# Kernel optimization log

Measured on AMD Instinct MI355X. Metric: run time of the kernel, lower is better.

Reference implementation:

```python
import jax, jax.numpy as jnp
import numpy as np

B, T, D, H, HD, I = 256, 1, 2048, 16, 128, 5504
EPS = 1e-6
ROPE_THETA = 10000.0


def setup_inputs() -> dict:
    key = jax.random.key(0)
    ks = jax.random.split(key, 20)
    W = 0.02  # weight init scale
    hidden_states = jax.random.normal(ks[0], (B, T, D), jnp.float32)
    # RoPE tables for each batch element at a distinct decode position
    pos = jnp.arange(B, dtype=jnp.float32) % 4096.0
    inv_freq = 1.0 / (ROPE_THETA ** (jnp.arange(0, HD, 2, dtype=jnp.float32) / HD))
    ang = pos[:, None] * inv_freq[None, :]                      # [B, HD/2]
    emb = jnp.concatenate([ang, ang], axis=-1)                  # [B, HD]
    cos = jnp.cos(emb)[:, None, :]                              # [B, 1, HD]
    sin = jnp.sin(emb)[:, None, :]
    n = lambda k, s: jax.random.normal(k, s, jnp.float32) * W
    return {
        'hidden_states': hidden_states, 'cos': cos, 'sin': sin,
        'router_w': n(ks[1], (D,)), 'router_b': jnp.zeros((1,), jnp.float32),
        'ln1_w': jnp.ones((D,), jnp.float32), 'ln2_w': jnp.ones((D,), jnp.float32),
        'wq': n(ks[2], (D, D)), 'bq': jnp.zeros((D,), jnp.float32),
        'wk': n(ks[3], (D, D)), 'bk': jnp.zeros((D,), jnp.float32),
        'wv': n(ks[4], (D, D)), 'bv': jnp.zeros((D,), jnp.float32),
        'wo': n(ks[5], (D, D)),
        'w_gate': n(ks[6], (D, I)), 'w_up': n(ks[7], (D, I)), 'w_down': n(ks[8], (I, D)),
        'k_sel': 128,
    }


def _rms(x, w):
    v = jnp.mean(jnp.square(x), axis=-1, keepdims=True)
    return x * jax.lax.rsqrt(v + EPS) * w


def _rotate_half(x):
    x1, x2 = jnp.split(x, 2, axis=-1)
    return jnp.concatenate([-x2, x1], axis=-1)


def _decoder_layer(x, cs, sn, ln1_w, ln2_w, wq, bq, wk, bk, wv, bv, wo, w_gate, w_up, w_down):
    # x: [k, T, D]; cs/sn: [k, T, HD]
    k = x.shape[0]
    h = _rms(x, ln1_w)
    q = (h @ wq + bq).reshape(k, T, H, HD).transpose(0, 2, 1, 3)  # [k,H,T,HD]
    kk = (h @ wk + bk).reshape(k, T, H, HD).transpose(0, 2, 1, 3)
    v = (h @ wv + bv).reshape(k, T, H, HD).transpose(0, 2, 1, 3)
    c = cs[:, None, :, :]  # [k,1,T,HD]
    s = sn[:, None, :, :]
    q = q * c + _rotate_half(q) * s
    kk = kk * c + _rotate_half(kk) * s
    att = jnp.einsum('bhqd,bhkd->bhqk', q, kk) * (HD ** -0.5)
    p = jax.nn.softmax(att, axis=-1)  # T==1: trivial causal mask
    o = jnp.einsum('bhqk,bhkd->bhqd', p, v).transpose(0, 2, 1, 3).reshape(k, T, D) @ wo
    x = x + o
    h2 = _rms(x, ln2_w)
    mlp = (jax.nn.silu(h2 @ w_gate) * (h2 @ w_up)) @ w_down
    return x + mlp


def reference(hidden_states, cos, sin, router_w, router_b, ln1_w, ln2_w,
              wq, bq, wk, bk, wv, bv, wo, w_gate, w_up, w_down, k_sel):
    # causal router: linear D->1 scores per batch row (T==1 decode step)
    scores = hidden_states[:, 0, :] @ router_w + router_b[0]   # [B]
    probs = jax.nn.sigmoid(scores)
    _, sel_idx = jax.lax.top_k(probs, k_sel)                   # [k]
    x_sel = hidden_states[sel_idx]                             # gather [k,T,D]
    cs, sn = cos[sel_idx], sin[sel_idx]                        # [k,T,HD]
    x_out = _decoder_layer(x_sel, cs, sn, ln1_w, ln2_w, wq, bq, wk, bk,
                           wv, bv, wo, w_gate, w_up, w_down)
    return hidden_states.at[sel_idx].set(x_out)                # scatter back
```

## Files before the change

kernel.cpp:

```cpp
#include <hip/hip_runtime.h>
#include <hip/hip_bf16.h>
#include <stdint.h>


#define D_ 2048
#define I_ 5504
#define NROWS 256
#define KSEL 128

typedef __attribute__((ext_vector_type(8))) short short8;
typedef __attribute__((ext_vector_type(4))) float floatx4;

__device__ __forceinline__ unsigned short f2bf(float f) {
  union { float f; unsigned int u; } v; v.f = f;
  unsigned int r = (v.u + 0x7FFFu + ((v.u >> 16) & 1u)) >> 16;
  return (unsigned short)r;
}

__global__ void k_router(const float* __restrict__ hid, const float* __restrict__ rw,
                         const float* __restrict__ rb, float* __restrict__ scores) {
  int b = blockIdx.x, t = threadIdx.x;
  const float* x = hid + (size_t)b * D_;
  float s = 0.f;
  for (int i = t; i < D_; i += 256) s += x[i] * rw[i];
  for (int o = 32; o; o >>= 1) s += __shfl_down(s, o);
  __shared__ float red[4];
  if ((t & 63) == 0) red[t >> 6] = s;
  __syncthreads();
  if (t == 0) scores[b] = red[0] + red[1] + red[2] + red[3] + rb[0];
}

__global__ void k_select(const float* __restrict__ scores, const int* __restrict__ kptr,
                         int* __restrict__ sel, int* __restrict__ pos) {
  __shared__ float sv[NROWS];
  int t = threadIdx.x;
  sv[t] = scores[t];
  __syncthreads();
  float s = sv[t];
  int c = 0;
  for (int j = 0; j < NROWS; ++j) {
    float o = sv[j];
    c += (o > s) || (o == s && j < t);
  }
  int k = *kptr;
  if (c < k) sel[c] = t;
  pos[t] = (c < k) ? c : -1;
}

__global__ void k_rms1(const float* __restrict__ hid, const int* __restrict__ sel,
                       const float* __restrict__ ln1, const float* __restrict__ bv,
                       unsigned short* __restrict__ Hb, float* __restrict__ V,
                       float* __restrict__ X1) {
  int i = blockIdx.x, t = threadIdx.x;
  int r = sel[i];
  const float* x = hid + (size_t)r * D_;
  float xs[8]; float ss = 0.f;
#pragma unroll
  for (int c = 0; c < 8; ++c) { float v = x[t + c * 256]; xs[c] = v; ss += v * v; }
  for (int o = 32; o; o >>= 1) ss += __shfl_down(ss, o);
  __shared__ float red[4];
  if ((t & 63) == 0) red[t >> 6] = ss;
  __syncthreads();
  float inv = rsqrtf((red[0] + red[1] + red[2] + red[3]) * (1.0f / D_) + 1e-6f);
#pragma unroll
  for (int c = 0; c < 8; ++c) {
    int idx = t + c * 256;
    size_t o_ = (size_t)i * D_ + idx;
    Hb[o_] = f2bf(xs[c] * inv * ln1[idx]);
    V[o_] = bv[idx];
    X1[o_] = xs[c];
  }
}

__global__ void k_rms2(const float* __restrict__ X1, const float* __restrict__ ln2,
                       unsigned short* __restrict__ H2b, float* __restrict__ G,
                       float* __restrict__ U) {
  int i = blockIdx.x, t = threadIdx.x;
  const float* x = X1 + (size_t)i * D_;
  float xs[8]; float ss = 0.f;
#pragma unroll
  for (int c = 0; c < 8; ++c) { float v = x[t + c * 256]; xs[c] = v; ss += v * v; }
  for (int o = 32; o; o >>= 1) ss += __shfl_down(ss, o);
  __shared__ float red[4];
  if ((t & 63) == 0) red[t >> 6] = ss;
  __syncthreads();
  float inv = rsqrtf((red[0] + red[1] + red[2] + red[3]) * (1.0f / D_) + 1e-6f);
#pragma unroll
  for (int c = 0; c < 8; ++c) {
    int idx = t + c * 256;
    H2b[(size_t)i * D_ + idx] = f2bf(xs[c] * inv * ln2[idx]);
  }
  for (int j = t; j < I_; j += 256) {
    G[(size_t)i * I_ + j] = 0.f;
    U[(size_t)i * I_ + j] = 0.f;
  }
}

__global__ void k_silu_out(const float* __restrict__ G, const float* __restrict__ U,
                           unsigned short* __restrict__ Mb,
                           const float* __restrict__ X1, const int* __restrict__ pos,
                           const float* __restrict__ hid, float* __restrict__ out) {
  int tid = blockIdx.x * 256 + threadIdx.x;
  int stride = gridDim.x * 256;
  const int nM = KSEL * I_;
  for (int i = tid; i < nM; i += stride) {
    float g = G[i], u = U[i];
    float m = (g / (1.f + expf(-g))) * u;
    Mb[i] = f2bf(m);
  }
  const int nO4 = NROWS * (D_ / 4);
  const float4* X14 = (const float4*)X1;
  const float4* H4 = (const float4*)hid;
  float4* O4 = (float4*)out;
  for (int i = tid; i < nO4; i += stride) {
    int row = i >> 9;
    int c4 = i & 511;
    int p = pos[row];
    O4[i] = (p >= 0) ? X14[(size_t)p * 512 + c4] : H4[i];
  }
}

template<bool AF32, bool DUAL>
__global__ __launch_bounds__(256)
void k_gemm(const void* __restrict__ Ap, const float* __restrict__ B0,
            const float* __restrict__ B1, float* __restrict__ C0,
            float* __restrict__ C1, const int* __restrict__ rowmap,
            int K, int N, int KT, int ldc) {
  constexpr int SA = 40;
  constexpr int SB = 40;
  const int bn = blockIdx.x;
  const int kt0 = blockIdx.y * KT;
  const int kt1 = min(K, kt0 + KT);
  const int tid = threadIdx.x;
  const int lane = tid & 63;
  const int wave = tid >> 6;
  const int wm = wave >> 1, wn = wave & 1;
  const int fm = lane & 15, kq = lane >> 4;

  __shared__ alignas(16) unsigned short Asm[128 * SA];
  __shared__ alignas(16) unsigned short Bsm0[64 * SB];
  __shared__ alignas(16) unsigned short Bsm1[DUAL ? 64 * SB : 8];

  floatx4 acc0[4][2] = {};
  floatx4 acc1[4][2] = {};

  const int ar = tid >> 1;
  const int ac = (tid & 1) * 16;
  const int n2 = (tid & 31) * 2;
  const int kh = (tid >> 5) * 4;

  const unsigned short* Ab = AF32 ? nullptr : (const unsigned short*)Ap + (size_t)ar * K + ac;
  const float*          Af = AF32 ? (const float*)Ap + (size_t)ar * K + ac : nullptr;
  const float* B0b = B0 + (size_t)bn * 64 + n2;
  const float* B1b = DUAL ? B1 + (size_t)bn * 64 + n2 : nullptr;

  uint4 a16[2];
  float af32[16];
  float2 b0r[4], b1r[4];

  auto load_tile = [&](int kt) {
    if (AF32) {
#pragma unroll
      for (int r = 0; r < 4; ++r)
        *(float4*)&af32[r * 4] = *(const float4*)(Af + kt + r * 4);
    } else {
      const uint4* Ag = (const uint4*)(Ab + kt);
      a16[0] = Ag[0]; a16[1] = Ag[1];
    }
    const float* Bg0 = B0b + (size_t)(kt + kh) * N;
#pragma unroll
    for (int r = 0; r < 4; ++r) b0r[r] = *(const float2*)(Bg0 + (size_t)r * N);
    if (DUAL) {
      const float* Bg1 = B1b + (size_t)(kt + kh) * N;
#pragma unroll
      for (int r = 0; r < 4; ++r) b1r[r] = *(const float2*)(Bg1 + (size_t)r * N);
    }
  };

  load_tile(kt0);

  for (int kt = kt0; kt < kt1; kt += 32) {
    __syncthreads();
    if (AF32) {
      alignas(16) unsigned short us[16];
#pragma unroll
      for (int r = 0; r < 16; ++r) us[r] = f2bf(af32[r]);
      uint4* Ad = (uint4*)&Asm[ar * SA + ac];
      Ad[0] = ((const uint4*)us)[0]; Ad[1] = ((const uint4*)us)[1];
    } else {
      uint4* Ad = (uint4*)&Asm[ar * SA + ac];
      Ad[0] = a16[0]; Ad[1] = a16[1];
    }
    {
      unsigned long long w0 = (unsigned long long)f2bf(b0r[0].x)
                            | ((unsigned long long)f2bf(b0r[1].x) << 16)
                            | ((unsigned long long)f2bf(b0r[2].x) << 32)
                            | ((unsigned long long)f2bf(b0r[3].x) << 48);
      unsigned long long w1 = (unsigned long long)f2bf(b0r[0].y)
                            | ((unsigned long long)f2bf(b0r[1].y) << 16)
                            | ((unsigned long long)f2bf(b0r[2].y) << 32)
                            | ((unsigned long long)f2bf(b0r[3].y) << 48);
      *(unsigned long long*)&Bsm0[(n2 + 0) * SB + kh] = w0;
      *(unsigned long long*)&Bsm0[(n2 + 1) * SB + kh] = w1;
      if (DUAL) {
        unsigned long long v0 = (unsigned long long)f2bf(b1r[0].x)
                              | ((unsigned long long)f2bf(b1r[1].x) << 16)
                              | ((unsigned long long)f2bf(b1r[2].x) << 32)
                              | ((unsigned long long)f2bf(b1r[3].x) << 48);
        unsigned long long v1 = (unsigned long long)f2bf(b1r[0].y)
                              | ((unsigned long long)f2bf(b1r[1].y) << 16)
                              | ((unsigned long long)f2bf(b1r[2].y) << 32)
                              | ((unsigned long long)f2bf(b1r[3].y) << 48);
        *(unsigned long long*)&Bsm1[(n2 + 0) * SB + kh] = v0;
        *(unsigned long long*)&Bsm1[(n2 + 1) * SB + kh] = v1;
      }
    }
    __syncthreads();
    if (kt + 32 < kt1) load_tile(kt + 32);
    short8 afr[4], bf0[2], bf1[2];
#pragma unroll
    for (int i = 0; i < 4; ++i)
      afr[i] = *(const short8*)&Asm[(wm * 64 + i * 16 + fm) * SA + kq * 8];
#pragma unroll
    for (int j = 0; j < 2; ++j)
      bf0[j] = *(const short8*)&Bsm0[(wn * 32 + j * 16 + fm) * SB + kq * 8];
    if (DUAL) {
#pragma unroll
      for (int j = 0; j < 2; ++j)
        bf1[j] = *(const short8*)&Bsm1[(wn * 32 + j * 16 + fm) * SB + kq * 8];
    }
#pragma unroll
    for (int i = 0; i < 4; ++i) {
#pragma unroll
      for (int j = 0; j < 2; ++j) {
        acc0[i][j] = __builtin_amdgcn_mfma_f32_16x16x32_bf16(afr[i], bf0[j], acc0[i][j], 0, 0, 0);
        if (DUAL)
          acc1[i][j] = __builtin_amdgcn_mfma_f32_16x16x32_bf16(afr[i], bf1[j], acc1[i][j], 0, 0, 0);
      }
    }
  }

#pragma unroll
  for (int i = 0; i < 4; ++i) {
#pragma unroll
    for (int r = 0; r < 4; ++r) {
      int row = wm * 64 + i * 16 + kq * 4 + r;
      size_t rbase = rowmap ? (size_t)rowmap[row] * ldc : (size_t)row * ldc;
#pragma unroll
      for (int j = 0; j < 2; ++j) {
        int col = bn * 64 + wn * 32 + j * 16 + fm;
        atomicAdd(&C0[rbase + col], acc0[i][j][r]);
        if (DUAL) atomicAdd(&C1[rbase + col], acc1[i][j][r]);
      }
    }
  }
}

extern "C" void kernel_launch(void* const* d_in, const int* in_sizes, int n_in,
                              void* d_out, int out_size, void* d_ws, size_t ws_size,
                              hipStream_t stream) {
  const float* hid = (const float*)d_in[0];
  const float* rw  = (const float*)d_in[3];
  const float* rb  = (const float*)d_in[4];
  const float* ln1 = (const float*)d_in[5];
  const float* ln2 = (const float*)d_in[6];
  const float* wv  = (const float*)d_in[11];
  const float* bv  = (const float*)d_in[12];
  const float* wo  = (const float*)d_in[13];
  const float* wg  = (const float*)d_in[14];
  const float* wu  = (const float*)d_in[15];
  const float* wd  = (const float*)d_in[16];
  const int*   kp  = (const int*)d_in[17];
  float* out = (float*)d_out;

  char* ws = (char*)d_ws;
  float*          scores = (float*)(ws + 0);
  int*            sel    = (int*)(ws + 1024);
  int*            pos    = (int*)(ws + 1536);
  unsigned short* Hb     = (unsigned short*)(ws + 4096);
  float*          V      = (float*)(ws + 528384);
  float*          X1     = (float*)(ws + 1576960);
  unsigned short* H2b    = (unsigned short*)(ws + 2625536);
  float*          G      = (float*)(ws + 3149824);
  float*          U      = (float*)(ws + 5967872);
  unsigned short* Mb     = (unsigned short*)(ws + 8785920);

  k_router<<<256, 256, 0, stream>>>(hid, rw, rb, scores);
  k_select<<<1, 256, 0, stream>>>(scores, kp, sel, pos);
  k_rms1<<<128, 256, 0, stream>>>(hid, sel, ln1, bv, Hb, V, X1);
  k_gemm<false, false><<<dim3(32, 8), 256, 0, stream>>>(Hb, wv, nullptr, V, nullptr, nullptr, 2048, 2048, 256, 2048);
  k_gemm<true, false><<<dim3(32, 8), 256, 0, stream>>>(V, wo, nullptr, X1, nullptr, nullptr, 2048, 2048, 256, 2048);
  k_rms2<<<128, 256, 0, stream>>>(X1, ln2, H2b, G, U);
  k_gemm<false, true><<<dim3(86, 4), 256, 0, stream>>>(H2b, wg, wu, G, U, nullptr, 2048, 5504, 512, 5504);
  k_silu_out<<<1024, 256, 0, stream>>>(G, U, Mb, X1, pos, hid, out);
  k_gemm<false, false><<<dim3(32, 8), 256, 0, stream>>>(Mb, wd, nullptr, out, nullptr, sel, 5504, 2048, 704, 2048);
}
```

Baseline: 318.7 us.

## Retile GEMM to 128x32 output with 64-deep K steps and packed bf16 conversion

The GEMM kernel shrinks the N tile from 64 to 32 columns and doubles the K step to 64, which doubles the grid and gives each thread eight K-consecutive B loads that pack into one 16-byte LDS store. Conversion now uses a packed bf16x2 intrinsic, and tile-boundary masking is added so K no longer has to divide evenly. The aim is more blocks in flight, higher occupancy (launch_bounds 256,2) and better overlap when streaming the fp32 weights. The trade-offs are that A is reloaded twice as many times, the B global loads become scalar strided accesses, and bounds checks are added.

Result: faster. 295.1 us (-7.4%).

```diff
diff --git a/kernel.cpp b/kernel.cpp
--- a/kernel.cpp
+++ b/kernel.cpp
@@ -15,6 +15,11 @@
   union { float f; unsigned int u; } v; v.f = f;
   unsigned int r = (v.u + 0x7FFFu + ((v.u >> 16) & 1u)) >> 16;
   return (unsigned short)r;
+}
+
+__device__ __forceinline__ unsigned int pk2(float lo, float hi) {
+  __hip_bfloat162 h = __float22bfloat162_rn(float2{lo, hi});
+  unsigned int u; __builtin_memcpy(&u, &h, 4); return u;
 }
 
 __global__ void k_router(const float* __restrict__ hid, const float* __restrict__ rw,
@@ -121,121 +126,116 @@
 }
 
 template<bool AF32, bool DUAL>
-__global__ __launch_bounds__(256)
+__global__ __launch_bounds__(256, 2)
 void k_gemm(const void* __restrict__ Ap, const float* __restrict__ B0,
             const float* __restrict__ B1, float* __restrict__ C0,
             float* __restrict__ C1, const int* __restrict__ rowmap,
-            int K, int N, int KT, int ldc) {
-  constexpr int SA = 40;
-  constexpr int SB = 40;
+            int K, int KA, int Kb, int lda, int N, int KT, int ldc) {
+  constexpr int ST = 72;
   const int bn = blockIdx.x;
   const int kt0 = blockIdx.y * KT;
-  const int kt1 = min(K, kt0 + KT);
+  const int kt1 = kt0 + KT;
   const int tid = threadIdx.x;
   const int lane = tid & 63;
   const int wave = tid >> 6;
   const int wm = wave >> 1, wn = wave & 1;
   const int fm = lane & 15, kq = lane >> 4;
 
-  __shared__ alignas(16) unsigned short Asm[128 * SA];
-  __shared__ alignas(16) unsigned short Bsm0[64 * SB];
-  __shared__ alignas(16) unsigned short Bsm1[DUAL ? 64 * SB : 8];
-
-  floatx4 acc0[4][2] = {};
-  floatx4 acc1[4][2] = {};
+  __shared__ alignas(16) unsigned short Asm[128 * ST];
+  __shared__ alignas(16) unsigned short Bsm0[32 * ST];
+  __shared__ alignas(16) unsigned short Bsm1[DUAL ? 32 * ST : 8];
+
+  floatx4 acc0[4] = {};
+  floatx4 acc1[4] = {};
 
   const int ar = tid >> 1;
-  const int ac = (tid & 1) * 16;
-  const int n2 = (tid & 31) * 2;
-  const int kh = (tid >> 5) * 4;
-
-  const unsigned short* Ab = AF32 ? nullptr : (const unsigned short*)Ap + (size_t)ar * K + ac;
-  const float*          Af = AF32 ? (const float*)Ap + (size_t)ar * K + ac : nullptr;
-  const float* B0b = B0 + (size_t)bn * 64 + n2;
-  const float* B1b = DUAL ? B1 + (size_t)bn * 64 + n2 : nullptr;
-
-  uint4 a16[2];
-  float af32[16];
-  float2 b0r[4], b1r[4];
+  const int ah = (tid & 1) * 32;
+  const int bnn = tid & 31;
+  const int bk8 = (tid >> 5) * 8;
+
+  const unsigned short* Ab = AF32 ? nullptr : (const unsigned short*)Ap + (size_t)ar * lda + ah;
+  const float*          Af = AF32 ? (const float*)Ap + (size_t)ar * lda + ah : nullptr;
+  const float* B0c = B0 + (size_t)(bn * 32 + bnn);
+  const float* B1c = DUAL ? B1 + (size_t)(bn * 32 + bnn) : nullptr;
+
+  uint4 a4[4];
+  float4 af8[8];
+  float b0v[8], b1v[8];
 
   auto load_tile = [&](int kt) {
     if (AF32) {
 #pragma unroll
-      for (int r = 0; r < 4; ++r)
-        *(float4*)&af32[r * 4] = *(const float4*)(Af + kt + r * 4);
+      for (int r = 0; r < 8; ++r) {
+        int c0 = kt + ah + r * 4;
+        af8[r] = (c0 < KA) ? *(const float4*)(Af + kt + r * 4)
+                           : make_float4(0.f, 0.f, 0.f, 0.f);
+      }
     } else {
-      const uint4* Ag = (const uint4*)(Ab + kt);
-      a16[0] = Ag[0]; a16[1] = Ag[1];
-    }
-    const float* Bg0 = B0b + (size_t)(kt + kh) * N;
-#pragma unroll
-    for (int r = 0; r < 4; ++r) b0r[r] = *(const float2*)(Bg0 + (size_t)r * N);
-    if (DUAL) {
-      const float* Bg1 = B1b + (size_t)(kt + kh) * N;
-#pragma unroll
-      for (int r = 0; r < 4; ++r) b1r[r] = *(const float2*)(Bg1 + (size_t)r * N);
+#pragma unroll
+      for (int r = 0; r < 4; ++r) {
+        int c0 = kt + ah + r * 8;
+        a4[r] = (c0 < KA) ? *(const uint4*)(Ab + kt + r * 8)
+                          : make_uint4(0u, 0u, 0u, 0u);
+      }
+    }
+#pragma unroll
+    for (int j = 0; j < 8; ++j) {
+      int kr = kt + bk8 + j; kr = kr < Kb ? kr : Kb - 1;
+      b0v[j] = B0c[(size_t)kr * N];
+      if (DUAL) b1v[j] = B1c[(size_t)kr * N];
     }
   };
 
   load_tile(kt0);
 
-  for (int kt = kt0; kt < kt1; kt += 32) {
+  for (int kt = kt0; kt < kt1; kt += 64) {
     __syncthreads();
-    if (AF32) {
-      alignas(16) unsigned short us[16];
-#pragma unroll
-      for (int r = 0; r < 16; ++r) us[r] = f2bf(af32[r]);
-      uint4* Ad = (uint4*)&Asm[ar * SA + ac];
-      Ad[0] = ((const uint4*)us)[0]; Ad[1] = ((const uint4*)us)[1];
-    } else {
-      uint4* Ad = (uint4*)&Asm[ar * SA + ac];
-      Ad[0] = a16[0]; Ad[1] = a16[1];
-    }
     {
-      unsigned long long w0 = (unsigned long long)f2bf(b0r[0].x)
-                            | ((unsigned long long)f2bf(b0r[1].x) << 16)
-                            | ((unsigned long long)f2bf(b0r[2].x) << 32)
-                            | ((unsigned long long)f2bf(b0r[3].x) << 48);
-      unsigned long long w1 = (unsigned long long)f2bf(b0r[0].y)
-                            | ((unsigned long long)f2bf(b0r[1].y) << 16)
-                            | ((unsigned long long)f2bf(b0r[2].y) << 32)
-                            | ((unsigned long long)f2bf(b0r[3].y) << 48);
-      *(unsigned long long*)&Bsm0[(n2 + 0) * SB + kh] = w0;
-      *(unsigned long long*)&Bsm0[(n2 + 1) * SB + kh] = w1;
+      uint4* Ad = (uint4*)&Asm[ar * ST + ah];
+      if (AF32) {
+        uint4 q;
+#pragma unroll
+        for (int r = 0; r < 4; ++r) {
+          q.x = pk2(af8[2 * r].x, af8[2 * r].y);
+          q.y = pk2(af8[2 * r].z, af8[2 * r].w);
+          q.z = pk2(af8[2 * r + 1].x, af8[2 * r + 1].y);
+          q.w = pk2(af8[2 * r + 1].z, af8[2 * r + 1].w);
+          Ad[r] = q;
+        }
+      } else {
+#pragma unroll
+        for (int r = 0; r < 4; ++r) Ad[r] = a4[r];
+      }
+      uint4 bq;
+      bq.x = pk2(b0v[0], b0v[1]); bq.y = pk2(b0v[2], b0v[3]);
+      bq.z = pk2(b0v[4], b0v[5]); bq.w = pk2(b0v[6], b0v[7]);
+      *(uint4*)&Bsm0[bnn * ST + bk8] = bq;
       if (DUAL) {
-        unsigned long long v0 = (unsigned long long)f2bf(b1r[0].x)
-                              | ((unsigned long long)f2bf(b1r[1].x) << 16)
-                              | ((unsigned long long)f2bf(b1r[2].x) << 32)
-                              | ((unsigned long long)f2bf(b1r[3].x) << 48);
-        unsigned long long v1 = (unsigned long long)f2bf(b1r[0].y)
-                              | ((unsigned long long)f2bf(b1r[1].y) << 16)
-                              | ((unsigned long long)f2bf(b1r[2].y) << 32)
-                              | ((unsigned long long)f2bf(b1r[3].y) << 48);
-        *(unsigned long long*)&Bsm1[(n2 + 0) * SB + kh] = v0;
-        *(unsigned long long*)&Bsm1[(n2 + 1) * SB + kh] = v1;
+        uint4 cq;
+        cq.x = pk2(b1v[0], b1v[1]); cq.y = pk2(b1v[2], b1v[3]);
+        cq.z = pk2(b1v[4], b1v[5]); cq.w = pk2(b1v[6], b1v[7]);
+        *(uint4*)&Bsm1[bnn * ST + bk8] = cq;
       }
     }
     __syncthreads();
-    if (kt + 32 < kt1) load_tile(kt + 32);
-    short8 afr[4], bf0[2], bf1[2];
-#pragma unroll
-    for (int i = 0; i < 4; ++i)
-      afr[i] = *(const short8*)&Asm[(wm * 64 + i * 16 + fm) * SA + kq * 8];
-#pragma unroll
-    for (int j = 0; j < 2; ++j)
-      bf0[j] = *(const short8*)&Bsm0[(wn * 32 + j * 16 + fm) * SB + kq * 8];
-    if (DUAL) {
-#pragma unroll
-      for (int j = 0; j < 2; ++j)
-        bf1[j] = *(const short8*)&Bsm1[(wn * 32 + j * 16 + fm) * SB + kq * 8];
-    }
-#pragma unroll
-    for (int i = 0; i < 4; ++i) {
-#pragma unroll
-      for (int j = 0; j < 2; ++j) {
-        acc0[i][j] = __builtin_amdgcn_mfma_f32_16x16x32_bf16(afr[i], bf0[j], acc0[i][j], 0, 0, 0);
+    if (kt + 64 < kt1) load_tile(kt + 64);
+    short8 afr[2][4], bf0[2], bf1[2];
+#pragma unroll
+    for (int s = 0; s < 2; ++s) {
+#pragma unroll
+      for (int i = 0; i < 4; ++i)
+        afr[s][i] = *(const short8*)&Asm[(wm * 64 + i * 16 + fm) * ST + s * 32 + kq * 8];
+      bf0[s] = *(const short8*)&Bsm0[(wn * 16 + fm) * ST + s * 32 + kq * 8];
+      if (DUAL)
+        bf1[s] = *(const short8*)&Bsm1[(wn * 16 + fm) * ST + s * 32 + kq * 8];
+    }
+#pragma unroll
+    for (int s = 0; s < 2; ++s) {
+#pragma unroll
+      for (int i = 0; i < 4; ++i) {
+        acc0[i] = __builtin_amdgcn_mfma_f32_16x16x32_bf16(afr[s][i], bf0[s], acc0[i], 0, 0, 0);
         if (DUAL)
-          acc1[i][j] = __builtin_amdgcn_mfma_f32_16x16x32_bf16(afr[i], bf1[j], acc1[i][j], 0, 0, 0);
+          acc1[i] = __builtin_amdgcn_mfma_f32_16x16x32_bf16(afr[s][i], bf1[s], acc1[i], 0, 0, 0);
       }
     }
   }
@@ -246,12 +246,9 @@
     for (int r = 0; r < 4; ++r) {
       int row = wm * 64 + i * 16 + kq * 4 + r;
       size_t rbase = rowmap ? (size_t)rowmap[row] * ldc : (size_t)row * ldc;
-#pragma unroll
-      for (int j = 0; j < 2; ++j) {
-        int col = bn * 64 + wn * 32 + j * 16 + fm;
-        atomicAdd(&C0[rbase + col], acc0[i][j][r]);
-        if (DUAL) atomicAdd(&C1[rbase + col], acc1[i][j][r]);
-      }
+      int col = bn * 32 + wn * 16 + fm;
+      atomicAdd(&C0[rbase + col], acc0[i][r]);
+      if (DUAL) atomicAdd(&C1[rbase + col], acc1[i][r]);
     }
   }
 }
@@ -288,10 +285,14 @@
   k_router<<<256, 256, 0, stream>>>(hid, rw, rb, scores);
   k_select<<<1, 256, 0, stream>>>(scores, kp, sel, pos);
   k_rms1<<<128, 256, 0, stream>>>(hid, sel, ln1, bv, Hb, V, X1);
-  k_gemm<false, false><<<dim3(32, 8), 256, 0, stream>>>(Hb, wv, nullptr, V, nullptr, nullptr, 2048, 2048, 256, 2048);
-  k_gemm<true, false><<<dim3(32, 8), 256, 0, stream>>>(V, wo, nullptr, X1, nullptr, nullptr, 2048, 2048, 256, 2048);
+  k_gemm<false, false><<<dim3(64, 8), 256, 0, stream>>>(
+      Hb, wv, nullptr, V, nullptr, nullptr, 2048, 2048, 2048, 2048, 2048, 256, 2048);
+  k_gemm<true, false><<<dim3(64, 8), 256, 0, stream>>>(
+      V, wo, nullptr, X1, nullptr, nullptr, 2048, 2048, 2048, 2048, 2048, 256, 2048);
   k_rms2<<<128, 256, 0, stream>>>(X1, ln2, H2b, G, U);
-  k_gemm<false, true><<<dim3(86, 4), 256, 0, stream>>>(H2b, wg, wu, G, U, nullptr, 2048, 5504, 512, 5504);
+  k_gemm<false, true><<<dim3(172, 4), 256, 0, stream>>>(
+      H2b, wg, wu, G, U, nullptr, 2048, 2048, 2048, 2048, 5504, 512, 5504);
   k_silu_out<<<1024, 256, 0, stream>>>(G, U, Mb, X1, pos, hid, out);
-  k_gemm<false, false><<<dim3(32, 8), 256, 0, stream>>>(Mb, wd, nullptr, out, nullptr, sel, 5504, 2048, 704, 2048);
-}
+  k_gemm<false, false><<<dim3(64, 8), 256, 0, stream>>>(
+      Mb, wd, nullptr, out, nullptr, sel, 5632, 5504, 5504, 5504, 2048, 704, 2048);
+}
```
